# Performance work log

Hardware: AMD Instinct MI355X
Metric: run time of the kernel (lower is better)

Reference implementation:

```python
import jax, jax.numpy as jnp
import numpy as np

M, NQ, NK, DZ, DX = 8, 1024, 1024, 256, 2
H, HD = 8, 32            # num_heads, head_dim
KH = 32                  # kernel MLP hidden width
INNER = H * HD           # 256


def setup_inputs() -> dict:
    key = jax.random.key(0)
    ks = jax.random.split(key, 12)
    f32 = jnp.float32
    return {
        "zq":  jax.random.normal(ks[0], (M, NQ, DZ), dtype=f32),
        "zk":  jax.random.normal(ks[1], (M, NK, DZ), dtype=f32),
        "zv":  jax.random.normal(ks[2], (M, NK, DZ), dtype=f32),
        "xq":  jax.random.normal(ks[3], (M, NQ, DX), dtype=f32),
        "xkv": jax.random.normal(ks[4], (M, NK, DX), dtype=f32),
        # projection weights (nn.Linear, bias=False); stored [in, out]
        "Wq":  jax.random.normal(ks[5], (DZ, INNER), dtype=f32) * 0.02,
        "Wk":  jax.random.normal(ks[6], (DZ, INNER), dtype=f32) * 0.02,
        "Wv":  jax.random.normal(ks[7], (DZ, INNER), dtype=f32) * 0.02,
        # output projection (Linear with bias; dropout p=0 -> identity)
        "Wout": jax.random.normal(ks[8], (INNER, DZ), dtype=f32) * 0.02,
        "bout": jnp.zeros((DZ,), dtype=f32),
        # kernel MLP: (dx + h) -> KH -> h
        "W1": jax.random.normal(ks[9], (DX + H, KH), dtype=f32) * 0.3,
        "b1": jnp.zeros((KH,), dtype=f32),
        "W2": jax.random.normal(ks[10], (KH, H), dtype=f32) * 0.3,
        "b2": jnp.zeros((H,), dtype=f32),
    }


def reference(zq, zk, zv, xq, xkv, Wq, Wk, Wv, Wout, bout, W1, b1, W2, b2):
    m, nq, _ = zq.shape
    nk = zk.shape[1]
    scale = HD ** -0.5

    # translation group action: pairwise position differences [m,nq,nk,dx]
    diff = xq[:, :, None, :] - xkv[:, None, :, :]

    q = (zq @ Wq).reshape(m, nq, H, HD)
    k = (zk @ Wk).reshape(m, nk, H, HD)
    v = (zv @ Wv).reshape(m, nk, H, HD)

    # token dots, already laid out as [m,nq,nk,h]
    token_dots = jnp.einsum("mqhd,mkhd->mqkh", q, k) * scale

    # kernel MLP over concatenated [diff, token_dots]: [m,nq,nk,dx+h] -> [m,nq,nk,h]
    kernel_input = jnp.concatenate([diff, token_dots], axis=-1)
    dots = jax.nn.relu(kernel_input @ W1 + b1) @ W2 + b2

    # softmax over keys (nk axis)
    attn = jax.nn.softmax(dots, axis=2)  # [m,nq,nk,h]

    out = jnp.einsum("mqkh,mkhd->mqhd", attn, v).reshape(m, nq, INNER)
    out = out @ Wout + bout

    # phi is None -> query locations pass through unchanged
    xq_new = xq
    return out, xq_new
```

## Files before the change

### kernel.cpp

```cpp
#include <hip/hip_runtime.h>

typedef float f32x4 __attribute__((ext_vector_type(4)));
typedef short s16x8 __attribute__((ext_vector_type(8)));
typedef unsigned short u16;
typedef unsigned int u32;

#define MFMA16 __builtin_amdgcn_mfma_f32_16x16x32_bf16
#define SCALE 0.17677669529663687f
#define LOG2E 1.44269504088896f

__device__ __forceinline__ u16 f2b(float f) {
  union { float f; unsigned u; } x; x.f = f;
  unsigned r = x.u + 0x7fffu + ((x.u >> 16) & 1u);
  return (u16)(r >> 16);
}
__device__ __forceinline__ float b2f(u16 s) {
  union { unsigned u; float f; } x; x.u = ((unsigned)s) << 16;
  return x.f;
}
__device__ __forceinline__ u32 pkt(float a, float b) {
  return __builtin_amdgcn_perm(__builtin_bit_cast(u32, b),
                               __builtin_bit_cast(u32, a), 0x07060302u);
}
__device__ __forceinline__ u32 bperm(int idx, u32 src) {
  return (u32)__builtin_amdgcn_ds_bpermute(idx, (int)src);
}
__device__ __forceinline__ s16x8 mk8(u32 a, u32 b, u32 c, u32 d) {
  union { u32 w[4]; s16x8 v; } u;
  u.w[0] = a; u.w[1] = b; u.w[2] = c; u.w[3] = d;
  return u.v;
}

__global__ __launch_bounds__(256) void wtrans_kernel(
    const float* __restrict__ Wq, const float* __restrict__ Wk,
    const float* __restrict__ Wv, const float* __restrict__ Wo,
    u16* __restrict__ WqT, u16* __restrict__ WkT,
    u16* __restrict__ WvT, u16* __restrict__ WoT) {
  const float* src; u16* dst;
  switch (blockIdx.x) {
    case 0: src = Wq; dst = WqT; break;
    case 1: src = Wk; dst = WkT; break;
    case 2: src = Wv; dst = WvT; break;
    default: src = Wo; dst = WoT; break;
  }
  int j = blockIdx.y;
  int d = threadIdx.x;
  dst[j * 256 + d] = f2b(src[d * 256 + j]);
}

__global__ __launch_bounds__(256) void copyxq_kernel(const float* __restrict__ xq,
                                                     float* __restrict__ dst) {
  int i = blockIdx.x * 256 + threadIdx.x;
  dst[i] = xq[i];
}

__global__ __launch_bounds__(256) void proj_kernel(
    const float* __restrict__ zq, const float* __restrict__ zk,
    const float* __restrict__ zv,
    const u16* __restrict__ WqT, const u16* __restrict__ WkT,
    const u16* __restrict__ WvT,
    u16* __restrict__ qb, u16* __restrict__ kb, u16* __restrict__ vT) {
  const int mat = blockIdx.z;
  const float* Z = (mat == 0) ? zq : (mat == 1) ? zk : zv;
  const u16* WT = (mat == 0) ? WqT : (mat == 1) ? WkT : WvT;
  const int n0 = blockIdx.x * 64;
  const int j0 = blockIdx.y * 64;
  const int tid = threadIdx.x;
  const int lane = tid & 63, wid = tid >> 6;
  const int l15 = lane & 15, lg = lane >> 4;
  const int wn = wid & 1, wj = wid >> 1;

  __shared__ u16 As[64][40];
  __shared__ u16 Bs[64][40];

  f32x4 acc[2][2];
  #pragma unroll
  for (int a = 0; a < 2; ++a)
    #pragma unroll
    for (int b = 0; b < 2; ++b) acc[a][b] = (f32x4){0.f, 0.f, 0.f, 0.f};

  for (int ks = 0; ks < 8; ++ks) {
    const int d0 = ks * 32;
    const int r = tid >> 2, cb = (tid & 3) * 8;
    const float* zsrc = &Z[(size_t)(n0 + r) * 256 + d0 + cb];
    s16x8 t;
    #pragma unroll
    for (int j = 0; j < 8; ++j) t[j] = (short)f2b(zsrc[j]);
    *(s16x8*)&As[r][cb] = t;
    *(s16x8*)&Bs[r][cb] = *(const s16x8*)&WT[(size_t)(j0 + r) * 256 + d0 + cb];
    __syncthreads();
    s16x8 a0 = *(const s16x8*)&As[wn * 32 + l15][lg * 8];
    s16x8 a1 = *(const s16x8*)&As[wn * 32 + 16 + l15][lg * 8];
    s16x8 b0 = *(const s16x8*)&Bs[wj * 32 + l15][lg * 8];
    s16x8 b1 = *(const s16x8*)&Bs[wj * 32 + 16 + l15][lg * 8];
    acc[0][0] = MFMA16(a0, b0, acc[0][0], 0, 0, 0);
    acc[0][1] = MFMA16(a0, b1, acc[0][1], 0, 0, 0);
    acc[1][0] = MFMA16(a1, b0, acc[1][0], 0, 0, 0);
    acc[1][1] = MFMA16(a1, b1, acc[1][1], 0, 0, 0);
    __syncthreads();
  }
  #pragma unroll
  for (int sn = 0; sn < 2; ++sn)
    #pragma unroll
    for (int sj = 0; sj < 2; ++sj)
      #pragma unroll
      for (int i = 0; i < 4; ++i) {
        int n = n0 + wn * 32 + sn * 16 + lg * 4 + i;
        int j = j0 + wj * 32 + sj * 16 + l15;
        float av = acc[sn][sj][i];
        if (mat == 0) av *= SCALE;
        u16 val = f2b(av);
        if (mat == 0) {
          qb[(size_t)n * 256 + j] = val;
        } else if (mat == 1) {
          kb[(size_t)n * 256 + j] = val;
        } else {
          int mm = n >> 10, nn = n & 1023;
          vT[((size_t)(mm * 256 + j)) * 1024 + nn] = val;
        }
      }
}

__global__ __launch_bounds__(512, 4) void attn_kernel(
    const u16* __restrict__ qb, const u16* __restrict__ kb,
    const u16* __restrict__ vT,
    const float* __restrict__ xq, const float* __restrict__ xkv,
    const float* __restrict__ W1, const float* __restrict__ b1,
    const float* __restrict__ W2, const float* __restrict__ b2,
    u16* __restrict__ preP, float* __restrict__ Lb) {
  const int bid = blockIdx.x;
  const int m = bid & 7;
  const int q0 = ((bid >> 3) & 63) * 16;
  const int kz = bid >> 9;
  const int tid = threadIdx.x;
  const int lane = tid & 63;
  const int wid = tid >> 6;
  const int l15 = lane & 15;
  const int lg = lane >> 4;
  const int kk = wid * 16 + l15;

  u16* myPre = preP + (size_t)kz * (8192 * 256);
  float* myL = Lb + (size_t)kz * (8192 * 8);

  __shared__ u16 P_s[8][16][128];

  s16x8 w1a[2];
  #pragma unroll
  for (int cblk = 0; cblk < 2; ++cblk) {
    const int c = 8 * (l15 >> 2) + 4 * cblk + (l15 & 3);
    #pragma unroll
    for (int j = 0; j < 8; ++j) {
      const int dim = lg * 8 + j;
      u16 v = 0;
      if (dim < 10) v = f2b(W1[dim * 32 + c]);
      else if (dim == 10) v = f2b(b1[c]);
      w1a[cblk][j] = (short)v;
    }
  }
  s16x8 w2a;
  #pragma unroll
  for (int j = 0; j < 8; ++j) {
    const int c = lg * 8 + j;
    w2a[j] = (short)((l15 < 8) ? f2b(W2[c * 8 + l15] * LOG2E) : (u16)0);
  }
  f32x4 b2v;
  #pragma unroll
  for (int i = 0; i < 4; ++i) b2v[i] = b2[(lg & 1) * 4 + i] * LOG2E;

  const int idx10 = (l15 + 0) * 4;
  const int idx11 = (l15 + 16) * 4;
  const int idx12 = (l15 + 32) * 4;
  const int idx13 = (l15 + 48) * 4;
  const u32 u1base = (lg == 1) ? 0x00003F80u : 0u;
  const bool lglo = (lg < 2);

  s16x8 ones;
  #pragma unroll
  for (int j = 0; j < 8; ++j) ones[j] = (l15 == 0) ? (short)0x3F80 : (short)0;

  s16x8 qfr[8];
  #pragma unroll
  for (int h = 0; h < 8; ++h)
    qfr[h] = *(const s16x8*)&qb[((size_t)(m * 1024 + q0 + l15)) * 256 + h * 32 + lg * 8];

  f32x4 acc_pv[2];
  acc_pv[0] = (f32x4){0.f, 0.f, 0.f, 0.f};
  acc_pv[1] = (f32x4){0.f, 0.f, 0.f, 0.f};
  f32x4 acc_sum = (f32x4){0.f, 0.f, 0.f, 0.f};
  const f32x4 Z4 = (f32x4){0.f, 0.f, 0.f, 0.f};

  for (int kt = 0; kt < 2; ++kt) {
    const int kg = kz * 256 + kt * 128;
    const float2 xk2 = *(const float2*)&xkv[((size_t)(m * 1024 + kg + kk)) * 2];

    u32 dpk[4][4];
    {
      f32x4 dacc[8];
      #pragma unroll
      for (int h = 0; h < 8; ++h) {
        const s16x8 b = *(const s16x8*)&kb[((size_t)(m * 1024 + kg + kk)) * 256 + h * 32 + lg * 8];
        dacc[h] = MFMA16(qfr[h], b, Z4, 0, 0, 0);
      }
      #pragma unroll
      for (int i = 0; i < 4; ++i)
        #pragma unroll
        for (int j = 0; j < 4; ++j)
          dpk[i][j] = pkt(dacc[2 * j][i], dacc[2 * j + 1][i]);
    }

    #pragma unroll 8
    for (int qg = 0; qg < 16; ++qg) {
      const int isrc = qg & 3;
      const int idxq = (qg >> 2) == 0 ? idx10 : (qg >> 2) == 1 ? idx11
                     : (qg >> 2) == 2 ? idx12 : idx13;
      const u32 p0 = bperm(idxq, dpk[isrc][0]);
      const u32 p1 = bperm(idxq, dpk[isrc][1]);
      const u32 p2 = bperm(idxq, dpk[isrc][2]);
      const u32 p3 = bperm(idxq, dpk[isrc][3]);
      const float2 xq2 = *(const float2*)&xq[((size_t)(m * 1024 + q0 + qg)) * 2];
      const u32 dqpair = pkt(xq2.x - xk2.x, xq2.y - xk2.y);
      const u32 u0 = (lg == 0) ? dqpair : ((lg == 1) ? p3 : 0u);
      const u32 u1 = (lg == 0) ? p0 : u1base;
      const u32 u2 = (lg == 0) ? p1 : 0u;
      const u32 u3 = (lg == 0) ? p2 : 0u;
      const s16x8 bf1 = mk8(u0, u1, u2, u3);
      const f32x4 h0 = MFMA16(w1a[0], bf1, Z4, 0, 0, 0);
      const f32x4 h1 = MFMA16(w1a[1], bf1, Z4, 0, 0, 0);
      const s16x8 bf2 = mk8(pkt(fmaxf(h0[0], 0.f), fmaxf(h0[1], 0.f)),
                            pkt(fmaxf(h0[2], 0.f), fmaxf(h0[3], 0.f)),
                            pkt(fmaxf(h1[0], 0.f), fmaxf(h1[1], 0.f)),
                            pkt(fmaxf(h1[2], 0.f), fmaxf(h1[3], 0.f)));
      const f32x4 Lg = MFMA16(w2a, bf2, b2v, 0, 0, 0);
      if (lglo) {
        #pragma unroll
        for (int i = 0; i < 4; ++i) {
          const float e = exp2f(Lg[i]);
          P_s[lg * 4 + i][qg][kk] = (u16)(__builtin_bit_cast(unsigned, e) >> 16);
        }
      }
    }
    __syncthreads();

    s16x8 pa[4];
    #pragma unroll
    for (int ks = 0; ks < 4; ++ks)
      pa[ks] = *(const s16x8*)&P_s[wid][l15][ks * 32 + lg * 8];
    #pragma unroll
    for (int dh = 0; dh < 2; ++dh) {
      const size_t vrow = ((size_t)(m * 256 + wid * 32 + dh * 16 + l15)) * 1024 + kg;
      #pragma unroll
      for (int ks = 0; ks < 4; ++ks) {
        const s16x8 b = *(const s16x8*)&vT[vrow + ks * 32 + lg * 8];
        acc_pv[dh] = MFMA16(pa[ks], b, acc_pv[dh], 0, 0, 0);
      }
    }
    #pragma unroll
    for (int ks = 0; ks < 4; ++ks)
      acc_sum = MFMA16(pa[ks], ones, acc_sum, 0, 0, 0);
    __syncthreads();
  }

  #pragma unroll
  for (int dh = 0; dh < 2; ++dh)
    #pragma unroll
    for (int i = 0; i < 4; ++i) {
      const int qr = lg * 4 + i;
      myPre[((size_t)(m * 1024 + q0 + qr)) * 256 + wid * 32 + dh * 16 + l15] = f2b(acc_pv[dh][i]);
    }
  if (l15 == 0) {
    #pragma unroll
    for (int i = 0; i < 4; ++i)
      myL[((size_t)(m * 1024 + q0 + lg * 4 + i)) * 8 + wid] = acc_sum[i];
  }
}

__global__ __launch_bounds__(256) void outp_kernel(
    const u16* __restrict__ preP, const float* __restrict__ Lb,
    const u16* __restrict__ WoT,
    const float* __restrict__ bout, float* __restrict__ out) {
  const int n0 = blockIdx.x * 64;
  const int j0 = blockIdx.y * 64;
  const int tid = threadIdx.x;
  const int lane = tid & 63, wid = tid >> 6;
  const int l15 = lane & 15, lg = lane >> 4;
  const int wn = wid & 1, wj = wid >> 1;
  __shared__ u16 As[64][40];
  __shared__ u16 Bs[64][40];
  f32x4 acc[2][2];
  #pragma unroll
  for (int a = 0; a < 2; ++a)
    #pragma unroll
    for (int b = 0; b < 2; ++b) acc[a][b] = (f32x4){0.f, 0.f, 0.f, 0.f};

  const size_t PSTRIDE = (size_t)8192 * 256;
  const size_t LSTRIDE = (size_t)8192 * 8;

  for (int ks = 0; ks < 8; ++ks) {
    const int d0 = ks * 32;
    const int r = tid >> 2, cb = (tid & 3) * 8;
    const size_t row = (size_t)(n0 + r);
    const float Ls = Lb[row * 8 + ks] + Lb[LSTRIDE + row * 8 + ks] +
                     Lb[2 * LSTRIDE + row * 8 + ks] + Lb[3 * LSTRIDE + row * 8 + ks];
    const float inv = 1.0f / Ls;
    const s16x8 p0 = *(const s16x8*)&preP[row * 256 + d0 + cb];
    const s16x8 p1 = *(const s16x8*)&preP[PSTRIDE + row * 256 + d0 + cb];
    const s16x8 p2 = *(const s16x8*)&preP[2 * PSTRIDE + row * 256 + d0 + cb];
    const s16x8 p3 = *(const s16x8*)&preP[3 * PSTRIDE + row * 256 + d0 + cb];
    s16x8 t;
    #pragma unroll
    for (int j = 0; j < 8; ++j) {
      const float v = (b2f((u16)p0[j]) + b2f((u16)p1[j]) + b2f((u16)p2[j]) + b2f((u16)p3[j])) * inv;
      t[j] = (short)f2b(v);
    }
    *(s16x8*)&As[r][cb] = t;
    *(s16x8*)&Bs[r][cb] = *(const s16x8*)&WoT[(size_t)(j0 + r) * 256 + d0 + cb];
    __syncthreads();
    s16x8 a0 = *(const s16x8*)&As[wn * 32 + l15][lg * 8];
    s16x8 a1 = *(const s16x8*)&As[wn * 32 + 16 + l15][lg * 8];
    s16x8 b0 = *(const s16x8*)&Bs[wj * 32 + l15][lg * 8];
    s16x8 b1 = *(const s16x8*)&Bs[wj * 32 + 16 + l15][lg * 8];
    acc[0][0] = MFMA16(a0, b0, acc[0][0], 0, 0, 0);
    acc[0][1] = MFMA16(a0, b1, acc[0][1], 0, 0, 0);
    acc[1][0] = MFMA16(a1, b0, acc[1][0], 0, 0, 0);
    acc[1][1] = MFMA16(a1, b1, acc[1][1], 0, 0, 0);
    __syncthreads();
  }
  #pragma unroll
  for (int sn = 0; sn < 2; ++sn)
    #pragma unroll
    for (int sj = 0; sj < 2; ++sj)
      #pragma unroll
      for (int i = 0; i < 4; ++i) {
        int n = n0 + wn * 32 + sn * 16 + lg * 4 + i;
        int j = j0 + wj * 32 + sj * 16 + l15;
        out[(size_t)n * 256 + j] = acc[sn][sj][i] + bout[j];
      }
}

extern "C" void kernel_launch(void* const* d_in, const int* in_sizes, int n_in,
                              void* d_out, int out_size, void* d_ws, size_t ws_size,
                              hipStream_t stream) {
  const float* zq = (const float*)d_in[0];
  const float* zk = (const float*)d_in[1];
  const float* zv = (const float*)d_in[2];
  const float* xq = (const float*)d_in[3];
  const float* xkv = (const float*)d_in[4];
  const float* Wq = (const float*)d_in[5];
  const float* Wk = (const float*)d_in[6];
  const float* Wv = (const float*)d_in[7];
  const float* Wo = (const float*)d_in[8];
  const float* bout = (const float*)d_in[9];
  const float* W1 = (const float*)d_in[10];
  const float* b1 = (const float*)d_in[11];
  const float* W2 = (const float*)d_in[12];
  const float* b2 = (const float*)d_in[13];
  float* out = (float*)d_out;

  const size_t MB = (size_t)1 << 20;
  char* ws = (char*)d_ws;
  u16* qb   = (u16*)(ws + 0 * MB);
  u16* kb   = (u16*)(ws + 4 * MB);
  u16* vT   = (u16*)(ws + 8 * MB);
  u16* preP = (u16*)(ws + 12 * MB);
  float* Lb = (float*)(ws + 28 * MB);
  u16* WqT  = (u16*)(ws + 29 * MB + 0 * (128 << 10));
  u16* WkT  = (u16*)(ws + 29 * MB + 1 * (128 << 10));
  u16* WvT  = (u16*)(ws + 29 * MB + 2 * (128 << 10));
  u16* WoT  = (u16*)(ws + 29 * MB + 3 * (128 << 10));

  wtrans_kernel<<<dim3(4, 256), dim3(256), 0, stream>>>(Wq, Wk, Wv, Wo, WqT, WkT, WvT, WoT);
  proj_kernel<<<dim3(128, 4, 3), dim3(256), 0, stream>>>(zq, zk, zv, WqT, WkT, WvT, qb, kb, vT);
  attn_kernel<<<dim3(2048), dim3(512), 0, stream>>>(qb, kb, vT, xq, xkv, W1, b1, W2, b2, preP, Lb);
  outp_kernel<<<dim3(128, 4), dim3(256), 0, stream>>>(preP, Lb, WoT, bout, out);
  copyxq_kernel<<<dim3(64), dim3(256), 0, stream>>>(xq, out + (size_t)8 * 1024 * 256);
}
```

Measured before the change: 152.7 us.

## Halve attention block to 4 waves, each handling two heads over 64-key tiles

The attention kernel now launches 256 threads per block instead of 512. Each wave loops over 64-key sub-tiles (four iterations instead of two) and accumulates PV for two heads instead of one. The shared P buffer shrinks to 64 keys per row plus padding. The aim is smaller blocks and less LDS so more blocks fit per CU, at the cost of more loop iterations and barriers. Part of the hidden loop body must also use the new key indexing, which is not visible here.

```diff
diff --git a/kernel.cpp b/kernel.cpp
--- a/kernel.cpp
+++ b/kernel.cpp
@@ -121,7 +121,7 @@
       }
 }
 
-__global__ __launch_bounds__(512, 4) void attn_kernel(
+__global__ __launch_bounds__(256, 4) void attn_kernel(
     const u16* __restrict__ qb, const u16* __restrict__ kb,
     const u16* __restrict__ vT,
     const float* __restrict__ xq, const float* __restrict__ xkv,
@@ -142,7 +142,7 @@
   u16* myPre = preP + (size_t)kz * (8192 * 256);
   float* myL = Lb + (size_t)kz * (8192 * 8);
 
-  __shared__ u16 P_s[8][16][128];
+  __shared__ u16 P_s[8][16][72];
 
   s16x8 w1a[2];
   #pragma unroll
@@ -183,14 +183,18 @@
   for (int h = 0; h < 8; ++h)
     qfr[h] = *(const s16x8*)&qb[((size_t)(m * 1024 + q0 + l15)) * 256 + h * 32 + lg * 8];
 
-  f32x4 acc_pv[2];
-  acc_pv[0] = (f32x4){0.f, 0.f, 0.f, 0.f};
-  acc_pv[1] = (f32x4){0.f, 0.f, 0.f, 0.f};
-  f32x4 acc_sum = (f32x4){0.f, 0.f, 0.f, 0.f};
+  f32x4 acc_pv[2][2];
+  f32x4 acc_sum[2];
+  #pragma unroll
+  for (int hh = 0; hh < 2; ++hh) {
+    acc_pv[hh][0] = (f32x4){0.f, 0.f, 0.f, 0.f};
+    acc_pv[hh][1] = (f32x4){0.f, 0.f, 0.f, 0.f};
+    acc_sum[hh] = (f32x4){0.f, 0.f, 0.f, 0.f};
+  }
   const f32x4 Z4 = (f32x4){0.f, 0.f, 0.f, 0.f};
 
-  for (int kt = 0; kt < 2; ++kt) {
-    const int kg = kz * 256 + kt * 128;
+  for (int kt = 0; kt < 4; ++kt) {
+    const int kg = kz * 256 + kt * 64;
     const float2 xk2 = *(const float2*)&xkv[((size_t)(m * 1024 + kg + kk)) * 2];
 
     u32 dpk[4][4];
@@ -241,36 +245,45 @@
     }
     __syncthreads();
 
-    s16x8 pa[4];
-    #pragma unroll
-    for (int ks = 0; ks < 4; ++ks)
-      pa[ks] = *(const s16x8*)&P_s[wid][l15][ks * 32 + lg * 8];
-    #pragma unroll
-    for (int dh = 0; dh < 2; ++dh) {
-      const size_t vrow = ((size_t)(m * 256 + wid * 32 + dh * 16 + l15)) * 1024 + kg;
-      #pragma unroll
-      for (int ks = 0; ks < 4; ++ks) {
-        const s16x8 b = *(const s16x8*)&vT[vrow + ks * 32 + lg * 8];
-        acc_pv[dh] = MFMA16(pa[ks], b, acc_pv[dh], 0, 0, 0);
-      }
-    }
-    #pragma unroll
-    for (int ks = 0; ks < 4; ++ks)
-      acc_sum = MFMA16(pa[ks], ones, acc_sum, 0, 0, 0);
-    __syncthreads();
-  }
-
-  #pragma unroll
-  for (int dh = 0; dh < 2; ++dh)
-    #pragma unroll
-    for (int i = 0; i < 4; ++i) {
-      const int qr = lg * 4 + i;
-      myPre[((size_t)(m * 1024 + q0 + qr)) * 256 + wid * 32 + dh * 16 + l15] = f2b(acc_pv[dh][i]);
-    }
-  if (l15 == 0) {
-    #pragma unroll
-    for (int i = 0; i < 4; ++i)
-      myL[((size_t)(m * 1024 + q0 + lg * 4 + i)) * 8 + wid] = acc_sum[i];
+    #pragma unroll
+    for (int hh = 0; hh < 2; ++hh) {
+      const int h = wid * 2 + hh;
+      s16x8 pa[2];
+      #pragma unroll
+      for (int ks = 0; ks < 2; ++ks)
+        pa[ks] = *(const s16x8*)&P_s[h][l15][ks * 32 + lg * 8];
+      #pragma unroll
+      for (int dh = 0; dh < 2; ++dh) {
+        const size_t vrow = ((size_t)(m * 256 + h * 32 + dh * 16 + l15)) * 1024 + kg;
+        #pragma unroll
+        for (int ks = 0; ks < 2; ++ks) {
+          const s16x8 b = *(const s16x8*)&vT[vrow + ks * 32 + lg * 8];
+          acc_pv[hh][dh] = MFMA16(pa[ks], b, acc_pv[hh][dh], 0, 0, 0);
+        }
+      }
+      #pragma unroll
+      for (int ks = 0; ks < 2; ++ks)
+        acc_sum[hh] = MFMA16(pa[ks], ones, acc_sum[hh], 0, 0, 0);
+    }
+    __syncthreads();
+  }
+
+  #pragma unroll
+  for (int hh = 0; hh < 2; ++hh) {
+    const int h = wid * 2 + hh;
+    #pragma unroll
+    for (int dh = 0; dh < 2; ++dh)
+      #pragma unroll
+      for (int i = 0; i < 4; ++i) {
+        const int qr = lg * 4 + i;
+        myPre[((size_t)(m * 1024 + q0 + qr)) * 256 + h * 32 + dh * 16 + l15] =
+            f2b(acc_pv[hh][dh][i]);
+      }
+    if (l15 == 0) {
+      #pragma unroll
+      for (int i = 0; i < 4; ++i)
+        myL[((size_t)(m * 1024 + q0 + lg * 4 + i)) * 8 + h] = acc_sum[hh][i];
+    }
   }
 }
 
@@ -370,7 +383,7 @@
 
   wtrans_kernel<<<dim3(4, 256), dim3(256), 0, stream>>>(Wq, Wk, Wv, Wo, WqT, WkT, WvT, WoT);
   proj_kernel<<<dim3(128, 4, 3), dim3(256), 0, stream>>>(zq, zk, zv, WqT, WkT, WvT, qb, kb, vT);
-  attn_kernel<<<dim3(2048), dim3(512), 0, stream>>>(qb, kb, vT, xq, xkv, W1, b1, W2, b2, preP, Lb);
+  attn_kernel<<<dim3(2048), dim3(256), 0, stream>>>(qb, kb, vT, xq, xkv, W1, b1, W2, b2, preP, Lb);
   outp_kernel<<<dim3(128, 4), dim3(256), 0, stream>>>(preP, Lb, WoT, bout, out);
   copyxq_kernel<<<dim3(64), dim3(256), 0, stream>>>(xq, out + (size_t)8 * 1024 * 256);
 }
```

Result: faster. 140.2 us (-8.2%).
